# Optimization experiments

Measured on AMD Instinct MI355X. Metric: run time of the kernel, lower is better.

Reference implementation:

```python
import jax, jax.numpy as jnp
import numpy as np

B, T, K = 256, 512, 128          # batch, seq_len, n_tag
START, STOP = 126, 127           # tag2idx[START_TAG], tag2idx[STOP_TAG]
NEG = -10000.0                   # same constant the torch module uses


def setup_inputs() -> dict:
    key = jax.random.key(0)
    k1, k2, k3 = jax.random.split(key, 3)
    feats = jax.random.normal(k1, (B, T, K), dtype=jnp.float32)
    tags = jax.random.randint(k2, (B, T), 0, 126)  # never START/STOP
    # learned CRF transition matrix: trans[to, from]
    transitions = 0.1 * jax.random.normal(k3, (K, K), dtype=jnp.float32)
    transitions = transitions.at[START, :].set(NEG).at[:, STOP].set(NEG)
    return {"feats": feats, "tags": tags, "transitions": transitions}


def _forward_alg(feats, trans):
    """Batched CRF forward algorithm. feats [B,T,K] -> log Z [B]."""
    b = feats.shape[0]
    init = jnp.full((b, K), NEG, feats.dtype).at[:, START].set(0.0)

    def step(alpha, feat_t):
        # scores[b, to, from] = alpha[b, from] + trans[to, from]
        scores = alpha[:, None, :] + trans[None, :, :]
        alpha_new = jax.nn.logsumexp(scores, axis=-1) + feat_t
        return alpha_new, None

    alpha, _ = jax.lax.scan(step, init, jnp.swapaxes(feats, 0, 1))
    return jax.nn.logsumexp(alpha + trans[STOP][None, :], axis=-1)


def _score_sentence(feats, tags, trans):
    """Batched gold path score. feats [B,T,K], tags [B,T] -> [B]."""
    b = feats.shape[0]
    start_col = jnp.full((b, 1), START, tags.dtype)
    tags_ext = jnp.concatenate([start_col, tags], axis=1)      # [B,T+1]
    trans_sc = trans[tags_ext[:, 1:], tags_ext[:, :-1]].sum(axis=1)
    emit_sc = jnp.take_along_axis(feats, tags[..., None], axis=2)[..., 0].sum(axis=1)
    return trans_sc + emit_sc + trans[STOP, tags[:, -1]]


def _viterbi(feats, trans):
    """Batched Viterbi decode. Returns (path_score [B], path [B,T])."""
    b = feats.shape[0]
    init = jnp.full((b, K), NEG, feats.dtype).at[:, START].set(0.0)

    def step(alpha, feat_t):
        scores = alpha[:, None, :] + trans[None, :, :]   # [B,to,from]
        bptr = jnp.argmax(scores, axis=-1)               # [B,to]
        alpha_new = jnp.max(scores, axis=-1) + feat_t
        return alpha_new, bptr

    alpha, bptrs = jax.lax.scan(step, init, jnp.swapaxes(feats, 0, 1))
    term = alpha + trans[STOP][None, :]
    last_tag = jnp.argmax(term, axis=-1)                 # [B]
    path_score = jnp.max(term, axis=-1)

    def back(tag_t, bp_t):
        prev = jnp.take_along_axis(bp_t, tag_t[:, None], axis=1)[:, 0]
        return prev, tag_t

    _, path = jax.lax.scan(back, last_tag, bptrs, reverse=True)  # [T,B]
    return path_score, jnp.swapaxes(path, 0, 1)


def reference(feats, tags, transitions):
    log_z = _forward_alg(feats, transitions)             # forward_alg per sentence
    gold = _score_sentence(feats, tags, transitions)     # score_sentence
    path_score, pred = _viterbi(feats, transitions)      # viterbi_decode
    loss = jnp.sum(log_z - gold) / jnp.float32(feats.shape[0] * feats.shape[1])
    return loss, path_score, pred
```

## Files before the change

kernel.cpp:

```cpp
#include <hip/hip_runtime.h>
#include <cstdint>
#include <cstddef>

#define BB 256
#define TT 512
#define KK 128
#define START_TAG 126
#define STOP_TAG 127
#define NEGV (-10000.0f)
#define NINF (-__builtin_huge_valf())

template<int CTRL>
__device__ __forceinline__ float dppf(float v, float old) {
  return __int_as_float(__builtin_amdgcn_update_dpp(
      __float_as_int(old), __float_as_int(v), CTRL, 0xf, 0xf, false));
}
template<int CTRL>
__device__ __forceinline__ int dppi(int v, int old) {
  return __builtin_amdgcn_update_dpp(old, v, CTRL, 0xf, 0xf, false);
}
__device__ __forceinline__ float wave_max63(float x) {
  x = fmaxf(x, dppf<0x111>(x, NINF));
  x = fmaxf(x, dppf<0x112>(x, NINF));
  x = fmaxf(x, dppf<0x114>(x, NINF));
  x = fmaxf(x, dppf<0x118>(x, NINF));
  x = fmaxf(x, dppf<0x142>(x, NINF));
  x = fmaxf(x, dppf<0x143>(x, NINF));
  return x;
}
__device__ __forceinline__ int paddr(int i) { return (i >> 5) * 36 + (i & 31); }

template<bool CHEAP>
__global__ __launch_bounds__(768) void crf_main(
    const float* __restrict__ feats, const float* __restrict__ trans,
    float* __restrict__ logz, float* __restrict__ pscore,
    int* __restrict__ lasttag, uint8_t* __restrict__ bptr,
    float* __restrict__ alphaS)
{
  const int b = blockIdx.x;
  const int tid = threadIdx.x;
  const bool is_fwd = tid < 256;
  const int lane = tid & 63;

  __shared__ __align__(16) float P[2][144];
  __shared__ __align__(16) float AV[2][144];
  __shared__ __align__(16) float redmF[2][4];
  __shared__ float reds[4];
  __shared__ float vitm[8];
  __shared__ int   viti[8];

  int myto, h;
  if (is_fwd) { myto = tid >> 1; h = tid & 1; }
  else { int q = tid - 256; myto = q >> 2; h = q & 3; }

  float R[64];
  if (is_fwd) {
    const float4* tr = (const float4*)(trans + (size_t)myto * KK + h * 64);
#pragma unroll
    for (int c = 0; c < 16; ++c) {
      float4 v = tr[c];
      R[4*c+0]=__expf(v.x); R[4*c+1]=__expf(v.y);
      R[4*c+2]=__expf(v.z); R[4*c+3]=__expf(v.w);
    }
  } else {
    const float4* tr = (const float4*)(trans + (size_t)myto * KK + h * 32);
#pragma unroll
    for (int c = 0; c < 8; ++c) {
      float4 v = tr[c];
      R[4*c+0]=v.x; R[4*c+1]=v.y; R[4*c+2]=v.z; R[4*c+3]=v.w;
    }
  }

  if (is_fwd) { if (h == 0) P[0][paddr(myto)] = (myto==START_TAG)?1.0f:0.0f; }
  else        { if (h == 0) AV[0][paddr(myto)] = (myto==START_TAG)?0.0f:NEGV; }
  if (tid < 4) redmF[1][tid] = 0.0f;
  __syncthreads();

  const float* fb = feats + (size_t)b * TT * KK + myto;
  uint8_t* bp = bptr + (size_t)b * TT * KK + myto;
  float* aS = alphaS + (size_t)b * TT * KK;

  float fcur = fb[0];
  float Mprev = 0.0f;
  float aCarry = 0.0f;
  int cur = 0;

  for (int t = 0; t < TT; ++t) {
    const int tn = (t + 1 < TT) ? t + 1 : t;
    float fnext = fb[(size_t)tn * KK];
    const int rd = (t + 1) & 1, wr = t & 1;

    if (is_fwd) {
      float4 rv = *(const float4*)&redmF[rd][0];
      float M1 = fmaxf(fmaxf(rv.x, rv.y), fmaxf(rv.z, rv.w));
      const float* Pc = &P[cur][0];
      const int base = h * 72;
      float s0=0.f, s1=0.f, s2=0.f, s3=0.f;
#pragma unroll
      for (int c = 0; c < 16; ++c) {
        float4 p = *(const float4*)&Pc[base + (c>>3)*36 + (c&7)*4];
        s0 = fmaf(R[4*c+0], p.x, s0);
        s1 = fmaf(R[4*c+1], p.y, s1);
        s2 = fmaf(R[4*c+2], p.z, s2);
        s3 = fmaf(R[4*c+3], p.w, s3);
      }
      float s = (s0 + s1) + (s2 + s3);
      s = s + dppf<0xB1>(s, s);
      float a;
      if (CHEAP) a = Mprev + __logf(s) + fcur;
      else       a = Mprev + logf(s) + fcur;
      float wm = wave_max63(a);
      if (lane == 63) redmF[wr][tid >> 6] = wm;
      float pv = CHEAP ? __expf(a - M1) : expf(a - M1);
      if (h == 0) P[cur ^ 1][paddr(myto)] = pv;
      Mprev = M1;
      aCarry = a;
    } else if (CHEAP) {
      const float* Ac = &AV[cur][0];
      const int base = h * 36;
      float4 p0 = *(const float4*)&Ac[base];
      float m0 = p0.x + R[0], m1 = p0.y + R[1];
      float m2 = p0.z + R[2], m3 = p0.w + R[3];
#pragma unroll
      for (int c = 1; c < 8; ++c) {
        float4 p = *(const float4*)&Ac[base + c*4];
        m0 = fmaxf(m0, p.x + R[4*c+0]);
        m1 = fmaxf(m1, p.y + R[4*c+1]);
        m2 = fmaxf(m2, p.z + R[4*c+2]);
        m3 = fmaxf(m3, p.w + R[4*c+3]);
      }
      float m = fmaxf(fmaxf(m0, m1), fmaxf(m2, m3));
      m = fmaxf(m, dppf<0xB1>(m, m));
      m = fmaxf(m, dppf<0x4E>(m, m));
      float a = m + fcur;
      if (h == 0) {
        AV[cur ^ 1][paddr(myto)] = a;
        __builtin_nontemporal_store(a, &aS[(size_t)t * KK + myto]);
      }
      aCarry = a;
    } else {
      const float* Ac = &AV[cur][0];
      const int base = h * 36;
      const int fb0 = h * 32;
      float4 p0 = *(const float4*)&Ac[base];
      float m0 = p0.x + R[0], m1 = p0.y + R[1], m2 = p0.z + R[2], m3 = p0.w + R[3];
      int i0 = fb0, i1 = fb0+1, i2 = fb0+2, i3 = fb0+3;
#pragma unroll
      for (int c = 1; c < 8; ++c) {
        float4 p = *(const float4*)&Ac[base + c*4];
        float v0 = p.x + R[4*c+0]; if (v0 > m0) { m0 = v0; i0 = fb0+4*c+0; }
        float v1 = p.y + R[4*c+1]; if (v1 > m1) { m1 = v1; i1 = fb0+4*c+1; }
        float v2 = p.z + R[4*c+2]; if (v2 > m2) { m2 = v2; i2 = fb0+4*c+2; }
        float v3 = p.w + R[4*c+3]; if (v3 > m3) { m3 = v3; i3 = fb0+4*c+3; }
      }
      float m = m0; int i = i0;
      if (m1 > m || (m1 == m && i1 < i)) { m = m1; i = i1; }
      if (m2 > m || (m2 == m && i2 < i)) { m = m2; i = i2; }
      if (m3 > m || (m3 == m && i3 < i)) { m = m3; i = i3; }
      { float mo = dppf<0xB1>(m, m); int io = dppi<0xB1>(i, i);
        if (mo > m || (mo == m && io < i)) { m = mo; i = io; } }
      { float mo = dppf<0x4E>(m, m); int io = dppi<0x4E>(i, i);
        if (mo > m || (mo == m && io < i)) { m = mo; i = io; } }
      float a = m + fcur;
      if (h == 0) { AV[cur ^ 1][paddr(myto)] = a; bp[(size_t)t * KK] = (uint8_t)i; }
      aCarry = a;
    }
    __syncthreads();
    cur ^= 1;
    fcur = fnext;
  }

  float tstop = trans[(size_t)STOP_TAG * KK + myto];
  float term = aCarry + tstop;
  float M = 0.0f;
  if (is_fwd) {
    float wm = wave_max63(term);
    if (lane == 63) redmF[0][tid >> 6] = wm;
  } else {
    float m = term; int i = myto;
#pragma unroll
    for (int off = 1; off < 64; off <<= 1) {
      float mo = __shfl_xor(m, off, 64);
      int   io = __shfl_xor(i, off, 64);
      if (mo > m || (mo == m && io < i)) { m = mo; i = io; }
    }
    if (lane == 0) { vitm[(tid>>6)-4] = m; viti[(tid>>6)-4] = i; }
  }
  __syncthreads();
  if (is_fwd) {
    float4 rv = *(const float4*)&redmF[0][0];
    M = fmaxf(fmaxf(rv.x, rv.y), fmaxf(rv.z, rv.w));
    float e = CHEAP ? __expf(term - M) : expf(term - M);
#pragma unroll
    for (int off = 1; off < 64; off <<= 1) e += __shfl_xor(e, off, 64);
    if (lane == 0) reds[tid >> 6] = e;
  } else if (tid == 256) {
    float m = vitm[0]; int i = viti[0];
#pragma unroll
    for (int w = 1; w < 8; ++w)
      if (vitm[w] > m || (vitm[w] == m && viti[w] < i)) { m = vitm[w]; i = viti[w]; }
    pscore[b] = m; lasttag[b] = i;
  }
  __syncthreads();
  if (tid == 0) {
    float sm = reds[0] + reds[1] + reds[2] + reds[3];
    logz[b] = M + (CHEAP ? __logf(sm) : logf(sm));
  }
}

__global__ __launch_bounds__(64) void backtrace_alpha(
    const float* __restrict__ alphaS, const float* __restrict__ trans,
    const int* __restrict__ lasttag, float* __restrict__ pred)
{
  const int b = blockIdx.x;
  const int lane = threadIdx.x;
  __shared__ float tl[KK * KK];
  {
    const float4* src = (const float4*)trans;
    float4* dst = (float4*)tl;
#pragma unroll
    for (int i = 0; i < (KK * KK / 4) / 64; ++i) dst[lane + i * 64] = src[lane + i * 64];
  }
  int tag = lasttag[b];
  if (lane == 0) pred[(size_t)b * TT + (TT - 1)] = (float)tag;
  const float* arow = alphaS + (size_t)b * TT * KK;

  float p0[8], p1[8];
#pragma unroll
  for (int j = 0; j < 8; ++j) {
    int r = TT - 2 - j;
    p0[j] = arow[(size_t)r * KK + lane];
    p1[j] = arow[(size_t)r * KK + 64 + lane];
  }
  __syncthreads();

  for (int rb = TT - 2; rb >= 0; rb -= 8) {
#pragma unroll
    for (int j = 0; j < 8; ++j) {
      int r = rb - j;
      if (r >= 0) {
        float x0 = p0[j] + tl[tag * KK + lane];
        float x1 = p1[j] + tl[tag * KK + 64 + lane];
        float m = fmaxf(x0, x1);
        float M = wave_max63(m);
        M = __int_as_float(__builtin_amdgcn_readlane(__float_as_int(M), 63));
        unsigned long long b0 = __ballot(x0 == M);
        unsigned long long b1 = __ballot(x1 == M);
        tag = b0 ? (int)__builtin_ctzll(b0) : 64 + (int)__builtin_ctzll(b1);
        if (lane == 0) pred[(size_t)b * TT + r] = (float)tag;
        int rp = r - 8;
        if (rp >= 0) {
          p0[j] = arow[(size_t)rp * KK + lane];
          p1[j] = arow[(size_t)rp * KK + 64 + lane];
        }
      }
    }
  }
}

__global__ __launch_bounds__(256) void backtrace_kernel(
    const uint8_t* __restrict__ bptr, const int* __restrict__ lasttag,
    float* __restrict__ pred)
{
  const int b = blockIdx.x;
  const int tid = threadIdx.x;
  __shared__ __align__(16) uint8_t lb[(TT / 2) * KK];
  __shared__ int tagcarry;
  if (tid == 0) tagcarry = lasttag[b];

  for (int half = 1; half >= 0; --half) {
    __syncthreads();
    const float4* src = reinterpret_cast<const float4*>(
        bptr + ((size_t)b * TT + (size_t)half * (TT / 2)) * KK);
    float4* dst = reinterpret_cast<float4*>(lb);
    for (int i = tid; i < (TT / 2) * KK / 16; i += 256) dst[i] = src[i];
    __syncthreads();
    if (tid == 0) {
      int tag = tagcarry;
      for (int t = TT / 2 - 1; t >= 0; --t) {
        int gt = half * (TT / 2) + t;
        pred[(size_t)b * TT + gt] = (float)tag;
        tag = lb[t * KK + tag];
      }
      tagcarry = tag;
    }
  }
}

__global__ __launch_bounds__(64) void gold_kernel(
    const float* __restrict__ feats, const int* __restrict__ tags,
    const float* __restrict__ trans, const float* __restrict__ logz,
    float* __restrict__ gb)
{
  const int b = blockIdx.x;
  const int lane = threadIdx.x;
  const int* tg = tags + (size_t)b * TT;
  const float* fb = feats + (size_t)b * TT * KK;
  float g = 0.0f;
#pragma unroll
  for (int k = 0; k < TT / 64; ++k) {
    int t = lane * (TT / 64) + k;
    int ct = tg[t];
    int pv = (t == 0) ? START_TAG : tg[t - 1];
    g += trans[ct * KK + pv] + fb[(size_t)t * KK + ct];
  }
  if (lane == 63) g += trans[STOP_TAG * KK + tg[TT - 1]];
#pragma unroll
  for (int off = 1; off <= 32; off <<= 1) g += __shfl_xor(g, off, 64);
  if (lane == 0) gb[b] = logz[b] - g;
}

__global__ __launch_bounds__(256) void loss_reduce(
    const float* __restrict__ gb, float* __restrict__ out)
{
  const int tid = threadIdx.x;
  const int lane = tid & 63, wv = tid >> 6;
  float v = gb[tid];
#pragma unroll
  for (int off = 1; off <= 32; off <<= 1) v += __shfl_xor(v, off, 64);
  __shared__ float red[4];
  if (lane == 0) red[wv] = v;
  __syncthreads();
  if (tid == 0) out[0] = (red[0] + red[1] + red[2] + red[3]) / (float)(BB * TT);
}

extern "C" void kernel_launch(void* const* d_in, const int* in_sizes, int n_in,
                              void* d_out, int out_size, void* d_ws, size_t ws_size,
                              hipStream_t stream) {
  const float* feats = (const float*)d_in[0];
  const int*   tags  = (const int*)d_in[1];
  const float* trans = (const float*)d_in[2];

  float* out    = (float*)d_out;
  float* loss   = out;
  float* pscore = out + 1;
  float* pred   = out + 1 + BB;
  (void)in_sizes; (void)n_in; (void)out_size;

  const size_t alpha_bytes = (size_t)BB * TT * KK * sizeof(float);
  const bool cheap = ws_size >= alpha_bytes + 4096;

  if (cheap) {
    float* alphaS  = (float*)d_ws;
    char*  wsend   = (char*)d_ws + alpha_bytes;
    float* logz    = (float*)(wsend);
    int*   lasttag = (int*)(wsend + BB * sizeof(float));
    float* gb      = (float*)(wsend + BB * sizeof(float) + BB * sizeof(int));
    crf_main<true><<<BB, 768, 0, stream>>>(feats, trans, logz, pscore, lasttag,
                                           (uint8_t*)nullptr, alphaS);
    backtrace_alpha<<<BB, 64, 0, stream>>>(alphaS, trans, lasttag, pred);
    gold_kernel<<<BB, 64, 0, stream>>>(feats, tags, trans, logz, gb);
    loss_reduce<<<1, 256, 0, stream>>>(gb, loss);
  } else {
    uint8_t* bptr    = (uint8_t*)d_ws;
    char*    wsend   = (char*)d_ws + (size_t)BB * TT * KK;
    float*   logz    = (float*)(wsend);
    int*     lasttag = (int*)(wsend + BB * sizeof(float));
    float*   gb      = (float*)(wsend + BB * sizeof(float) + BB * sizeof(int));
    crf_main<false><<<BB, 768, 0, stream>>>(feats, trans, logz, pscore, lasttag,
                                            bptr, (float*)nullptr);
    backtrace_kernel<<<BB, 256, 0, stream>>>(bptr, lasttag, pred);
    gold_kernel<<<BB, 64, 0, stream>>>(feats, tags, trans, logz, gb);
    loss_reduce<<<1, 256, 0, stream>>>(gb, loss);
  }
}
```

Before: 426.0 us.

## Fuse CRF forward, Viterbi and gold score with lazy rescaling in probability space

Rewrites the main kernel to use 512 threads. The forward pass now runs in linear probability space: each step is p_new = (expT · p) * exp(feat), and the running max is renormalised only once every 4 steps instead of taking a per-step log/exp and cross-wave max. The Viterbi half uses two threads per tag with v_max3 reductions and one DPP step. The gold-score computation is folded into the forward threads, and the loss reduction is folded into an extra block of the backtrace kernel, cutting two launches. The risk is float overflow or underflow between renormalisations, since exp(feat) growth goes unchecked for 4 steps, which changes numerical behaviour compared with the log-space version.

```diff
diff --git a/kernel.cpp b/kernel.cpp
--- a/kernel.cpp
+++ b/kernel.cpp
@@ -14,10 +14,6 @@
 __device__ __forceinline__ float dppf(float v, float old) {
   return __int_as_float(__builtin_amdgcn_update_dpp(
       __float_as_int(old), __float_as_int(v), CTRL, 0xf, 0xf, false));
-}
-template<int CTRL>
-__device__ __forceinline__ int dppi(int v, int old) {
-  return __builtin_amdgcn_update_dpp(old, v, CTRL, 0xf, 0xf, false);
 }
 __device__ __forceinline__ float wave_max63(float x) {
   x = fmaxf(x, dppf<0x111>(x, NINF));
@@ -28,192 +24,179 @@
   x = fmaxf(x, dppf<0x143>(x, NINF));
   return x;
 }
-__device__ __forceinline__ int paddr(int i) { return (i >> 5) * 36 + (i & 31); }
-
-template<bool CHEAP>
-__global__ __launch_bounds__(768) void crf_main(
+__device__ __forceinline__ float max3f(float a, float b, float c) {
+  float d;
+  asm("v_max3_f32 %0, %1, %2, %3" : "=v"(d) : "v"(a), "v"(b), "v"(c));
+  return d;
+}
+template<int N> struct ic { static constexpr int v = N; };
+
+__global__ __launch_bounds__(512) void crf_fused(
     const float* __restrict__ feats, const float* __restrict__ trans,
-    float* __restrict__ logz, float* __restrict__ pscore,
-    int* __restrict__ lasttag, uint8_t* __restrict__ bptr,
-    float* __restrict__ alphaS)
+    const int* __restrict__ tags,
+    float* __restrict__ pscore, int* __restrict__ lasttag,
+    float* __restrict__ alphaS, float* __restrict__ gb)
 {
   const int b = blockIdx.x;
   const int tid = threadIdx.x;
-  const bool is_fwd = tid < 256;
+  const bool isv = tid < 256;
+  const int lt  = isv ? tid : tid - 256;
+  const int to  = lt >> 1;
+  const int h   = lt & 1;
   const int lane = tid & 63;
 
-  __shared__ __align__(16) float P[2][144];
-  __shared__ __align__(16) float AV[2][144];
-  __shared__ __align__(16) float redmF[2][4];
-  __shared__ float reds[4];
-  __shared__ float vitm[8];
-  __shared__ int   viti[8];
-
-  int myto, h;
-  if (is_fwd) { myto = tid >> 1; h = tid & 1; }
-  else { int q = tid - 256; myto = q >> 2; h = q & 3; }
+  __shared__ __align__(16) float AV[2][KK];
+  __shared__ __align__(16) float P [2][KK];
+  __shared__ __align__(16) float pwm[4];
+  __shared__ float vitm[2]; __shared__ int viti[2];
+  __shared__ float reds[2]; __shared__ float redg[4];
 
   float R[64];
-  if (is_fwd) {
-    const float4* tr = (const float4*)(trans + (size_t)myto * KK + h * 64);
+  {
+    const float4* tr = (const float4*)(trans + (size_t)to * KK + h * 64);
 #pragma unroll
     for (int c = 0; c < 16; ++c) {
       float4 v = tr[c];
-      R[4*c+0]=__expf(v.x); R[4*c+1]=__expf(v.y);
-      R[4*c+2]=__expf(v.z); R[4*c+3]=__expf(v.w);
+      if (isv) { R[4*c+0]=v.x; R[4*c+1]=v.y; R[4*c+2]=v.z; R[4*c+3]=v.w; }
+      else     { R[4*c+0]=__expf(v.x); R[4*c+1]=__expf(v.y);
+                 R[4*c+2]=__expf(v.z); R[4*c+3]=__expf(v.w); }
+    }
+  }
+
+  if (tid < KK)                 AV[0][tid] = (tid == START_TAG) ? 0.0f : NEGV;
+  if (tid >= 256 && lt < KK)    P[0][lt]   = (lt == START_TAG) ? 1.0f : 0.0f;
+  __syncthreads();
+
+  const float* fb = feats + (size_t)b * TT * KK + to;
+  float* aSb = alphaS + (size_t)b * TT * KK + to;
+
+  float M = 0.0f;
+  float fcur = 0.f, fn = 0.f;
+  if (!isv || h == 0) { fcur = fb[0]; fn = fb[KK]; }
+
+  for (int t4 = 0; t4 < TT; t4 += 4) {
+    auto step = [&](auto phc) {
+      constexpr int PH = decltype(phc)::v;
+      const int t = t4 + PH;
+      const int tpf = (t + 2 < TT) ? t + 2 : TT - 1;
+      float f2 = 0.f;
+      if (!isv || h == 0) f2 = fb[(size_t)tpf * KK];
+
+      if (isv) {
+        const float* Ac = AV[PH & 1];
+        float4 p = *(const float4*)&Ac[h * 64];
+        float m0 = fmaxf(p.x + R[0], p.y + R[1]);
+        float m1 = fmaxf(p.z + R[2], p.w + R[3]);
+#pragma unroll
+        for (int c = 1; c < 16; ++c) {
+          p = *(const float4*)&Ac[h * 64 + c * 4];
+          m0 = max3f(m0, p.x + R[4*c+0], p.y + R[4*c+1]);
+          m1 = max3f(m1, p.z + R[4*c+2], p.w + R[4*c+3]);
+        }
+        float m = fmaxf(m0, m1);
+        m = fmaxf(m, dppf<0xB1>(m, m));
+        if (h == 0) {
+          float a = m + fcur;
+          AV[(PH & 1) ^ 1][to] = a;
+          __builtin_nontemporal_store(a, &aSb[(size_t)t * KK]);
+          fcur = fn; fn = f2;
+        }
+      } else {
+        float corr = 1.0f;
+        if (PH == 0 && t4) {
+          float4 pw = *(const float4*)pwm;
+          float pmax = fmaxf(fmaxf(pw.x, pw.y), fmaxf(pw.z, pw.w));
+          M += __logf(pmax);
+          corr = 1.0f / pmax;
+        }
+        const float* Pc = P[PH & 1];
+        float s0=0.f, s1=0.f, s2=0.f, s3=0.f;
+#pragma unroll
+        for (int c = 0; c < 16; ++c) {
+          float4 p = *(const float4*)&Pc[h * 64 + c * 4];
+          s0 = fmaf(R[4*c+0], p.x, s0);
+          s1 = fmaf(R[4*c+1], p.y, s1);
+          s2 = fmaf(R[4*c+2], p.z, s2);
+          s3 = fmaf(R[4*c+3], p.w, s3);
+        }
+        float s = (s0 + s1) + (s2 + s3);
+        s = s + dppf<0xB1>(s, s);
+        float ef = __expf(fcur);
+        if (PH == 0 && t4) ef *= corr;
+        float pv = s * ef;
+        if (h == 0) P[(PH & 1) ^ 1][to] = pv;
+        if (PH == 3) {
+          float wm = wave_max63(pv);
+          if (lane == 63) pwm[(tid >> 6) & 3] = wm;
+        }
+        fcur = fn; fn = f2;
+      }
+      __syncthreads();
+    };
+    step(ic<0>{}); step(ic<1>{}); step(ic<2>{}); step(ic<3>{});
+  }
+
+  if (isv) {
+    if (tid < KK) {
+      float term = AV[0][tid] + trans[(size_t)STOP_TAG * KK + tid];
+      float m = term; int i = tid;
+#pragma unroll
+      for (int off = 1; off < 64; off <<= 1) {
+        float mo = __shfl_xor(m, off, 64);
+        int   io = __shfl_xor(i, off, 64);
+        if (mo > m || (mo == m && io < i)) { m = mo; i = io; }
+      }
+      if (lane == 0) { vitm[tid >> 6] = m; viti[tid >> 6] = i; }
     }
   } else {
-    const float4* tr = (const float4*)(trans + (size_t)myto * KK + h * 32);
-#pragma unroll
-    for (int c = 0; c < 8; ++c) {
-      float4 v = tr[c];
-      R[4*c+0]=v.x; R[4*c+1]=v.y; R[4*c+2]=v.z; R[4*c+3]=v.w;
-    }
-  }
-
-  if (is_fwd) { if (h == 0) P[0][paddr(myto)] = (myto==START_TAG)?1.0f:0.0f; }
-  else        { if (h == 0) AV[0][paddr(myto)] = (myto==START_TAG)?0.0f:NEGV; }
-  if (tid < 4) redmF[1][tid] = 0.0f;
-  __syncthreads();
-
-  const float* fb = feats + (size_t)b * TT * KK + myto;
-  uint8_t* bp = bptr + (size_t)b * TT * KK + myto;
-  float* aS = alphaS + (size_t)b * TT * KK;
-
-  float fcur = fb[0];
-  float Mprev = 0.0f;
-  float aCarry = 0.0f;
-  int cur = 0;
-
-  for (int t = 0; t < TT; ++t) {
-    const int tn = (t + 1 < TT) ? t + 1 : t;
-    float fnext = fb[(size_t)tn * KK];
-    const int rd = (t + 1) & 1, wr = t & 1;
-
-    if (is_fwd) {
-      float4 rv = *(const float4*)&redmF[rd][0];
-      float M1 = fmaxf(fmaxf(rv.x, rv.y), fmaxf(rv.z, rv.w));
-      const float* Pc = &P[cur][0];
-      const int base = h * 72;
-      float s0=0.f, s1=0.f, s2=0.f, s3=0.f;
-#pragma unroll
-      for (int c = 0; c < 16; ++c) {
-        float4 p = *(const float4*)&Pc[base + (c>>3)*36 + (c&7)*4];
-        s0 = fmaf(R[4*c+0], p.x, s0);
-        s1 = fmaf(R[4*c+1], p.y, s1);
-        s2 = fmaf(R[4*c+2], p.z, s2);
-        s3 = fmaf(R[4*c+3], p.w, s3);
-      }
-      float s = (s0 + s1) + (s2 + s3);
-      s = s + dppf<0xB1>(s, s);
-      float a;
-      if (CHEAP) a = Mprev + __logf(s) + fcur;
-      else       a = Mprev + logf(s) + fcur;
-      float wm = wave_max63(a);
-      if (lane == 63) redmF[wr][tid >> 6] = wm;
-      float pv = CHEAP ? __expf(a - M1) : expf(a - M1);
-      if (h == 0) P[cur ^ 1][paddr(myto)] = pv;
-      Mprev = M1;
-      aCarry = a;
-    } else if (CHEAP) {
-      const float* Ac = &AV[cur][0];
-      const int base = h * 36;
-      float4 p0 = *(const float4*)&Ac[base];
-      float m0 = p0.x + R[0], m1 = p0.y + R[1];
-      float m2 = p0.z + R[2], m3 = p0.w + R[3];
-#pragma unroll
-      for (int c = 1; c < 8; ++c) {
-        float4 p = *(const float4*)&Ac[base + c*4];
-        m0 = fmaxf(m0, p.x + R[4*c+0]);
-        m1 = fmaxf(m1, p.y + R[4*c+1]);
-        m2 = fmaxf(m2, p.z + R[4*c+2]);
-        m3 = fmaxf(m3, p.w + R[4*c+3]);
-      }
-      float m = fmaxf(fmaxf(m0, m1), fmaxf(m2, m3));
-      m = fmaxf(m, dppf<0xB1>(m, m));
-      m = fmaxf(m, dppf<0x4E>(m, m));
-      float a = m + fcur;
-      if (h == 0) {
-        AV[cur ^ 1][paddr(myto)] = a;
-        __builtin_nontemporal_store(a, &aS[(size_t)t * KK + myto]);
-      }
-      aCarry = a;
-    } else {
-      const float* Ac = &AV[cur][0];
-      const int base = h * 36;
-      const int fb0 = h * 32;
-      float4 p0 = *(const float4*)&Ac[base];
-      float m0 = p0.x + R[0], m1 = p0.y + R[1], m2 = p0.z + R[2], m3 = p0.w + R[3];
-      int i0 = fb0, i1 = fb0+1, i2 = fb0+2, i3 = fb0+3;
-#pragma unroll
-      for (int c = 1; c < 8; ++c) {
-        float4 p = *(const float4*)&Ac[base + c*4];
-        float v0 = p.x + R[4*c+0]; if (v0 > m0) { m0 = v0; i0 = fb0+4*c+0; }
-        float v1 = p.y + R[4*c+1]; if (v1 > m1) { m1 = v1; i1 = fb0+4*c+1; }
-        float v2 = p.z + R[4*c+2]; if (v2 > m2) { m2 = v2; i2 = fb0+4*c+2; }
-        float v3 = p.w + R[4*c+3]; if (v3 > m3) { m3 = v3; i3 = fb0+4*c+3; }
-      }
-      float m = m0; int i = i0;
-      if (m1 > m || (m1 == m && i1 < i)) { m = m1; i = i1; }
-      if (m2 > m || (m2 == m && i2 < i)) { m = m2; i = i2; }
-      if (m3 > m || (m3 == m && i3 < i)) { m = m3; i = i3; }
-      { float mo = dppf<0xB1>(m, m); int io = dppi<0xB1>(i, i);
-        if (mo > m || (mo == m && io < i)) { m = mo; i = io; } }
-      { float mo = dppf<0x4E>(m, m); int io = dppi<0x4E>(i, i);
-        if (mo > m || (mo == m && io < i)) { m = mo; i = io; } }
-      float a = m + fcur;
-      if (h == 0) { AV[cur ^ 1][paddr(myto)] = a; bp[(size_t)t * KK] = (uint8_t)i; }
-      aCarry = a;
-    }
-    __syncthreads();
-    cur ^= 1;
-    fcur = fnext;
-  }
-
-  float tstop = trans[(size_t)STOP_TAG * KK + myto];
-  float term = aCarry + tstop;
-  float M = 0.0f;
-  if (is_fwd) {
-    float wm = wave_max63(term);
-    if (lane == 63) redmF[0][tid >> 6] = wm;
-  } else {
-    float m = term; int i = myto;
-#pragma unroll
-    for (int off = 1; off < 64; off <<= 1) {
-      float mo = __shfl_xor(m, off, 64);
-      int   io = __shfl_xor(i, off, 64);
-      if (mo > m || (mo == m && io < i)) { m = mo; i = io; }
-    }
-    if (lane == 0) { vitm[(tid>>6)-4] = m; viti[(tid>>6)-4] = i; }
-  }
-  __syncthreads();
-  if (is_fwd) {
-    float4 rv = *(const float4*)&redmF[0][0];
-    M = fmaxf(fmaxf(rv.x, rv.y), fmaxf(rv.z, rv.w));
-    float e = CHEAP ? __expf(term - M) : expf(term - M);
-#pragma unroll
-    for (int off = 1; off < 64; off <<= 1) e += __shfl_xor(e, off, 64);
-    if (lane == 0) reds[tid >> 6] = e;
-  } else if (tid == 256) {
-    float m = vitm[0]; int i = viti[0];
-#pragma unroll
-    for (int w = 1; w < 8; ++w)
-      if (vitm[w] > m || (vitm[w] == m && viti[w] < i)) { m = vitm[w]; i = viti[w]; }
-    pscore[b] = m; lasttag[b] = i;
+    if (lt < KK) {
+      float e = P[0][lt] * __expf(trans[(size_t)STOP_TAG * KK + lt]);
+#pragma unroll
+      for (int off = 1; off < 64; off <<= 1) e += __shfl_xor(e, off, 64);
+      if (lane == 0) reds[lt >> 6] = e;
+    }
+    const int* tg = tags + (size_t)b * TT;
+    const float* fg = feats + (size_t)b * TT * KK;
+    float g = 0.0f;
+#pragma unroll
+    for (int k2 = 0; k2 < 2; ++k2) {
+      int t = lt + k2 * 256;
+      int ct = tg[t];
+      int pv2 = (t == 0) ? START_TAG : tg[t - 1];
+      g += trans[(size_t)ct * KK + pv2] + fg[(size_t)t * KK + ct];
+      if (t == TT - 1) g += trans[(size_t)STOP_TAG * KK + ct];
+    }
+#pragma unroll
+    for (int off = 1; off < 64; off <<= 1) g += __shfl_xor(g, off, 64);
+    if (lane == 0) redg[(tid >> 6) & 3] = g;
   }
   __syncthreads();
   if (tid == 0) {
-    float sm = reds[0] + reds[1] + reds[2] + reds[3];
-    logz[b] = M + (CHEAP ? __logf(sm) : logf(sm));
-  }
-}
-
-__global__ __launch_bounds__(64) void backtrace_alpha(
+    float mm = vitm[0]; int ii = viti[0];
+    if (vitm[1] > mm || (vitm[1] == mm && viti[1] < ii)) { mm = vitm[1]; ii = viti[1]; }
+    pscore[b] = mm; lasttag[b] = ii;
+  }
+  if (tid == 256) {
+    float se = reds[0] + reds[1];
+    float sg = redg[0] + redg[1] + redg[2] + redg[3];
+    gb[b] = (M + __logf(se)) - sg;
+  }
+}
+
+__global__ __launch_bounds__(64) void backtrace_loss(
     const float* __restrict__ alphaS, const float* __restrict__ trans,
-    const int* __restrict__ lasttag, float* __restrict__ pred)
-{
+    const int* __restrict__ lasttag, const float* __restrict__ gb,
+    float* __restrict__ pred, float* __restrict__ loss_out)
+{
+  const int lane = threadIdx.x;
+  if (blockIdx.x == BB) {
+    float v = gb[lane] + gb[lane + 64] + gb[lane + 128] + gb[lane + 192];
+#pragma unroll
+    for (int off = 1; off < 64; off <<= 1) v += __shfl_xor(v, off, 64);
+    if (lane == 0) loss_out[0] = v / (float)(BB * TT);
+    return;
+  }
   const int b = blockIdx.x;
-  const int lane = threadIdx.x;
   __shared__ float tl[KK * KK];
   {
     const float4* src = (const float4*)trans;
@@ -258,6 +241,158 @@
   }
 }
 
+template<int CTRL>
+__device__ __forceinline__ int dppi(int v, int old) {
+  return __builtin_amdgcn_update_dpp(old, v, CTRL, 0xf, 0xf, false);
+}
+__device__ __forceinline__ int paddr(int i) { return (i >> 5) * 36 + (i & 31); }
+
+__global__ __launch_bounds__(768) void crf_main_fb(
+    const float* __restrict__ feats, const float* __restrict__ trans,
+    float* __restrict__ logz, float* __restrict__ pscore,
+    int* __restrict__ lasttag, uint8_t* __restrict__ bptr)
+{
+  const int b = blockIdx.x;
+  const int tid = threadIdx.x;
+  const bool is_fwd = tid < 256;
+  const int lane = tid & 63;
+
+  __shared__ __align__(16) float P[2][144];
+  __shared__ __align__(16) float AV[2][144];
+  __shared__ __align__(16) float redmF[2][4];
+  __shared__ float reds[4];
+  __shared__ float vitm[8];
+  __shared__ int   viti[8];
+
+  int myto, h;
+  if (is_fwd) { myto = tid >> 1; h = tid & 1; }
+  else { int q = tid - 256; myto = q >> 2; h = q & 3; }
+
+  float R[64];
+  if (is_fwd) {
+    const float4* tr = (const float4*)(trans + (size_t)myto * KK + h * 64);
+#pragma unroll
+    for (int c = 0; c < 16; ++c) {
+      float4 v = tr[c];
+      R[4*c+0]=expf(v.x); R[4*c+1]=expf(v.y); R[4*c+2]=expf(v.z); R[4*c+3]=expf(v.w);
+    }
+  } else {
+    const float4* tr = (const float4*)(trans + (size_t)myto * KK + h * 32);
+#pragma unroll
+    for (int c = 0; c < 8; ++c) {
+      float4 v = tr[c];
+      R[4*c+0]=v.x; R[4*c+1]=v.y; R[4*c+2]=v.z; R[4*c+3]=v.w;
+    }
+  }
+
+  if (is_fwd) { if (h == 0) P[0][paddr(myto)] = (myto==START_TAG)?1.0f:0.0f; }
+  else        { if (h == 0) AV[0][paddr(myto)] = (myto==START_TAG)?0.0f:NEGV; }
+  if (tid < 4) redmF[1][tid] = 0.0f;
+  __syncthreads();
+
+  const float* fb = feats + (size_t)b * TT * KK + myto;
+  uint8_t* bp = bptr + (size_t)b * TT * KK + myto;
+
+  float fcur = fb[0];
+  float Mprev = 0.0f;
+  float aCarry = 0.0f;
+  int cur = 0;
+
+  for (int t = 0; t < TT; ++t) {
+    const int tn = (t + 1 < TT) ? t + 1 : t;
+    float fnext = fb[(size_t)tn * KK];
+    const int rd = (t + 1) & 1, wr = t & 1;
+
+    if (is_fwd) {
+      float4 rv = *(const float4*)&redmF[rd][0];
+      float M1 = fmaxf(fmaxf(rv.x, rv.y), fmaxf(rv.z, rv.w));
+      const float* Pc = &P[cur][0];
+      const int base = h * 72;
+      float s0=0.f, s1=0.f, s2=0.f, s3=0.f;
+#pragma unroll
+      for (int c = 0; c < 16; ++c) {
+        float4 p = *(const float4*)&Pc[base + (c>>3)*36 + (c&7)*4];
+        s0 = fmaf(R[4*c+0], p.x, s0);
+        s1 = fmaf(R[4*c+1], p.y, s1);
+        s2 = fmaf(R[4*c+2], p.z, s2);
+        s3 = fmaf(R[4*c+3], p.w, s3);
+      }
+      float s = (s0 + s1) + (s2 + s3);
+      s = s + dppf<0xB1>(s, s);
+      float a = Mprev + logf(s) + fcur;
+      float wm = wave_max63(a);
+      if (lane == 63) redmF[wr][tid >> 6] = wm;
+      float pv = expf(a - M1);
+      if (h == 0) P[cur ^ 1][paddr(myto)] = pv;
+      Mprev = M1;
+      aCarry = a;
+    } else {
+      const float* Ac = &AV[cur][0];
+      const int base = h * 36;
+      const int fb0 = h * 32;
+      float4 p0 = *(const float4*)&Ac[base];
+      float m0 = p0.x + R[0], m1 = p0.y + R[1], m2 = p0.z + R[2], m3 = p0.w + R[3];
+      int i0 = fb0, i1 = fb0+1, i2 = fb0+2, i3 = fb0+3;
+#pragma unroll
+      for (int c = 1; c < 8; ++c) {
+        float4 p = *(const float4*)&Ac[base + c*4];
+        float v0 = p.x + R[4*c+0]; if (v0 > m0) { m0 = v0; i0 = fb0+4*c+0; }
+        float v1 = p.y + R[4*c+1]; if (v1 > m1) { m1 = v1; i1 = fb0+4*c+1; }
+        float v2 = p.z + R[4*c+2]; if (v2 > m2) { m2 = v2; i2 = fb0+4*c+2; }
+        float v3 = p.w + R[4*c+3]; if (v3 > m3) { m3 = v3; i3 = fb0+4*c+3; }
+      }
+      float m = m0; int i = i0;
+      if (m1 > m || (m1 == m && i1 < i)) { m = m1; i = i1; }
+      if (m2 > m || (m2 == m && i2 < i)) { m = m2; i = i2; }
+      if (m3 > m || (m3 == m && i3 < i)) { m = m3; i = i3; }
+      { float mo = dppf<0xB1>(m, m); int io = dppi<0xB1>(i, i);
+        if (mo > m || (mo == m && io < i)) { m = mo; i = io; } }
+      { float mo = dppf<0x4E>(m, m); int io = dppi<0x4E>(i, i);
+        if (mo > m || (mo == m && io < i)) { m = mo; i = io; } }
+      float a = m + fcur;
+      if (h == 0) { AV[cur ^ 1][paddr(myto)] = a; bp[(size_t)t * KK] = (uint8_t)i; }
+      aCarry = a;
+    }
+    __syncthreads();
+    cur ^= 1;
+    fcur = fnext;
+  }
+
+  float tstop = trans[(size_t)STOP_TAG * KK + myto];
+  float term = aCarry + tstop;
+  float M = 0.0f;
+  if (is_fwd) {
+    float wm = wave_max63(term);
+    if (lane == 63) redmF[0][tid >> 6] = wm;
+  } else {
+    float m = term; int i = myto;
+#pragma unroll
+    for (int off = 1; off < 64; off <<= 1) {
+      float mo = __shfl_xor(m, off, 64);
+      int   io = __shfl_xor(i, off, 64);
+      if (mo > m || (mo == m && io < i)) { m = mo; i = io; }
+    }
+    if (lane == 0) { vitm[(tid>>6)-4] = m; viti[(tid>>6)-4] = i; }
+  }
+  __syncthreads();
+  if (is_fwd) {
+    float4 rv = *(const float4*)&redmF[0][0];
+    M = fmaxf(fmaxf(rv.x, rv.y), fmaxf(rv.z, rv.w));
+    float e = (h == 0) ? expf(term - M) : 0.0f;
+#pragma unroll
+    for (int off = 1; off < 64; off <<= 1) e += __shfl_xor(e, off, 64);
+    if (lane == 0) reds[tid >> 6] = e;
+  } else if (tid == 256) {
+    float m = vitm[0]; int i = viti[0];
+#pragma unroll
+    for (int w = 1; w < 8; ++w)
+      if (vitm[w] > m || (vitm[w] == m && viti[w] < i)) { m = vitm[w]; i = viti[w]; }
+    pscore[b] = m; lasttag[b] = i;
+  }
+  __syncthreads();
+  if (tid == 0) logz[b] = M + logf(reds[0] + reds[1] + reds[2] + reds[3]);
+}
+
 __global__ __launch_bounds__(256) void backtrace_kernel(
     const uint8_t* __restrict__ bptr, const int* __restrict__ lasttag,
     float* __restrict__ pred)
@@ -343,22 +478,19 @@
   if (cheap) {
     float* alphaS  = (float*)d_ws;
     char*  wsend   = (char*)d_ws + alpha_bytes;
-    float* logz    = (float*)(wsend);
-    int*   lasttag = (int*)(wsend + BB * sizeof(float));
-    float* gb      = (float*)(wsend + BB * sizeof(float) + BB * sizeof(int));
-    crf_main<true><<<BB, 768, 0, stream>>>(feats, trans, logz, pscore, lasttag,
-                                           (uint8_t*)nullptr, alphaS);
-    backtrace_alpha<<<BB, 64, 0, stream>>>(alphaS, trans, lasttag, pred);
-    gold_kernel<<<BB, 64, 0, stream>>>(feats, tags, trans, logz, gb);
-    loss_reduce<<<1, 256, 0, stream>>>(gb, loss);
+    int*   lasttag = (int*)(wsend);
+    float* gb      = (float*)(wsend + BB * sizeof(int));
+    crf_fused<<<BB, 512, 0, stream>>>(feats, trans, tags, pscore, lasttag,
+                                      alphaS, gb);
+    backtrace_loss<<<BB + 1, 64, 0, stream>>>(alphaS, trans, lasttag, gb,
+                                              pred, loss);
   } else {
     uint8_t* bptr    = (uint8_t*)d_ws;
     char*    wsend   = (char*)d_ws + (size_t)BB * TT * KK;
     float*   logz    = (float*)(wsend);
     int*     lasttag = (int*)(wsend + BB * sizeof(float));
     float*   gb      = (float*)(wsend + BB * sizeof(float) + BB * sizeof(int));
-    crf_main<false><<<BB, 768, 0, stream>>>(feats, trans, logz, pscore, lasttag,
-                                            bptr, (float*)nullptr);
+    crf_main_fb<<<BB, 768, 0, stream>>>(feats, trans, logz, pscore, lasttag, bptr);
     backtrace_kernel<<<BB, 256, 0, stream>>>(bptr, lasttag, pred);
     gold_kernel<<<BB, 64, 0, stream>>>(feats, tags, trans, logz, gb);
     loss_reduce<<<1, 256, 0, stream>>>(gb, loss);
```

Result: slower. 504.6 us (+18.5%).
